# Kernel optimization log

Measured on AMD Instinct MI355X. Metric: run time of the kernel, lower is better.

Reference implementation:

```python
import jax, jax.numpy as jnp
import numpy as np

B, T = 16384, 79
DIMS = [(1, 64), (64, 32), (32, 16), (16, 8), (8, 16), (16, 32), (32, 64), (64, 79)]


def _simple_rnn(x, Wx, Wh, b, act, return_seq):
    # x: [B, T, D] -> SimpleRNN: h_t = act(x_t @ Wx + h_{t-1} @ Wh + b)
    xb = jnp.einsum('btd,du->btu', x, Wx) + b  # precompute input projection
    h0 = jnp.zeros((x.shape[0], Wh.shape[0]), x.dtype)

    def step(h, xt):
        h = act(xt + h @ Wh)
        return h, h

    hT, hs = jax.lax.scan(step, h0, jnp.swapaxes(xb, 0, 1))  # scan over time
    return jnp.swapaxes(hs, 0, 1) if return_seq else hT


def setup_inputs() -> dict:
    key = jax.random.key(0)
    ks = jax.random.split(key, 3 * len(DIMS) + 1)
    inp = {"x": jax.random.normal(ks[0], (B, T), dtype=jnp.float32)}
    for i, (d, u) in enumerate(DIMS):
        inp[f"Wx{i}"] = jax.random.normal(ks[1 + 3 * i], (d, u), dtype=jnp.float32) / np.sqrt(d).astype(np.float32)
        inp[f"Wh{i}"] = jax.random.normal(ks[2 + 3 * i], (u, u), dtype=jnp.float32) / np.sqrt(u).astype(np.float32)
        inp[f"b{i}"] = jnp.zeros((u,), dtype=jnp.float32)
    return inp


def reference(x, Wx0, Wh0, b0, Wx1, Wh1, b1, Wx2, Wh2, b2, Wx3, Wh3, b3,
              Wx4, Wh4, b4, Wx5, Wh5, b5, Wx6, Wh6, b6, Wx7, Wh7, b7):
    params = [(Wx0, Wh0, b0), (Wx1, Wh1, b1), (Wx2, Wh2, b2), (Wx3, Wh3, b3),
              (Wx4, Wh4, b4), (Wx5, Wh5, b5), (Wx6, Wh6, b6), (Wx7, Wh7, b7)]
    h = x[..., None]  # [B, T, 1]  (tf.expand_dims(x, -1))
    n = len(params)
    for i, (Wx, Wh, b) in enumerate(params):
        last = i == n - 1
        act = jax.nn.sigmoid if last else jax.nn.relu
        h = _simple_rnn(h, Wx, Wh, b, act, return_seq=not last)
    return h  # decoded: [B, 79]
```

## Files before the change

### kernel.cpp

```cpp
#include <hip/hip_runtime.h>
#include <hip/hip_bf16.h>

#define DEVFN static __device__ __forceinline__

typedef short bf16x8 __attribute__((ext_vector_type(8)));
typedef float f32x4  __attribute__((ext_vector_type(4)));

constexpr int TSEQ  = 79;
constexpr int NSTEP = TSEQ + 7;
constexpr int MWG   = 16;
constexpr int ROWU  = 344;
constexpr int NBLK  = 16384 / MWG;

constexpr int LD[8]   = {1,64,32,16,8,16,32,64};
constexpr int LU[8]   = {64,32,16,8,16,32,64,79};
constexpr int LS[8]   = {0,8,72,104,120,128,144,176};
constexpr int LO[8]   = {8,72,104,120,128,144,176,240};
constexpr int LKP[8]  = {96,96,64,32,32,64,96,160};
constexpr int LKS[8]  = {3,3,2,1,1,2,3,5};
constexpr int LUP[8]  = {64,32,16,16,16,32,64,80};
constexpr int WOFF[8] = {0,6144,9216,10240,10752,11264,13312,19456};
constexpr int WTOTAL  = 32256;

constexpr int WNG[4]     = {1,2,4,2};
constexpr int WGL[4][4]  = {{7,0,0,0},{7,1,0,0},{0,2,3,4},{6,5,0,0}};
constexpr int WGT0[4][4] = {{0,0,0,0},{3,0,0,0},{0,0,0,0},{0,0,0,0}};
constexpr int WGNT[4][4] = {{3,0,0,0},{2,2,0,0},{4,1,1,1},{4,2,0,0}};

DEVFN unsigned short f2bf(float f) {
  unsigned int u = __builtin_bit_cast(unsigned int, f);
  unsigned int r = (u + 0x7FFFu + ((u >> 16) & 1u)) >> 16;
  return (unsigned short)r;
}
DEVFN unsigned int pkbf(float a, float b) {
#if __has_builtin(__builtin_amdgcn_cvt_pk_bf16_f32)
  auto r = __builtin_amdgcn_cvt_pk_bf16_f32(a, b);
  static_assert(sizeof(r) == 4, "v2bf16 expected");
  return __builtin_bit_cast(unsigned int, r);
#else
  return (unsigned)f2bf(a) | ((unsigned)f2bf(b) << 16);
#endif
}
DEVFN float sigmoidf(float v) { return 1.0f / (1.0f + __expf(-v)); }

__global__ void __launch_bounds__(256) prep_weights(
    const float* Wx0, const float* Wh0, const float* Wx1, const float* Wh1,
    const float* Wx2, const float* Wh2, const float* Wx3, const float* Wh3,
    const float* Wx4, const float* Wh4, const float* Wx5, const float* Wh5,
    const float* Wx6, const float* Wh6, const float* Wx7, const float* Wh7,
    unsigned short* __restrict__ wt)
{
  const float* wxp[8] = {Wx0,Wx1,Wx2,Wx3,Wx4,Wx5,Wx6,Wx7};
  const float* whp[8] = {Wh0,Wh1,Wh2,Wh3,Wh4,Wh5,Wh6,Wh7};
  int idx = blockIdx.x * 256 + threadIdx.x;
  if (idx >= WTOTAL) return;
#pragma unroll
  for (int l = 0; l < 8; ++l) {
    int sz = LUP[l] * LKP[l];
    if (idx >= WOFF[l] && idx < WOFF[l] + sz) {
      int local = idx - WOFF[l];
      int j = local / LKP[l];
      int k = local - j * LKP[l];
      float v = 0.f;
      if (j < LU[l]) {
        if (l == 0) {
          if (k == 0) v = Wx0[j];
          else if (k >= 8 && k < 72) v = Wh0[(k - 8) * 64 + j];
        } else {
          if (k < LD[l]) v = wxp[l][k * LU[l] + j];
          else if (k < LD[l] + LU[l]) v = whp[l][(k - LD[l]) * LU[l] + j];
        }
      }
      wt[idx] = f2bf(v);
    }
  }
}

template <int W>
DEVFN void preload(const unsigned short* __restrict__ wt, int lane, bf16x8 (&af)[16])
{
  const int m0 = lane & 15, quad = lane >> 4;
  int ai = 0;
#pragma unroll
  for (int g = 0; g < 4; ++g) {
    if (g >= WNG[W]) break;
    const int l = WGL[W][g], t0 = WGT0[W][g], nt = WGNT[W][g];
    const int ks = LKS[l], Kp = LKP[l];
#pragma unroll
    for (int t = 0; t < 4; ++t) {
      if (t >= nt) continue;
      const int j = (t0 + t) * 16 + m0;
      const unsigned short* base = wt + WOFF[l] + j * Kp;
#pragma unroll
      for (int k = 0; k < 5; ++k) {
        if (k >= ks) continue;
        af[ai + t * ks + k] = *reinterpret_cast<const bf16x8*>(base + k * 32 + quad * 8);
      }
    }
    ai += nt * ks;
  }
}

template <int W>
DEVFN void step(int s, const unsigned short (*rb)[ROWU], unsigned short (*wb)[ROWU],
                const bf16x8 (&af)[16], const float (*bl)[80],
                const unsigned short (*xl)[80], float* __restrict__ out,
                int bb, int lane)
{
  const int m = lane & 15, quad = lane >> 4;
  int ai = 0;
#pragma unroll
  for (int g = 0; g < 4; ++g) {
    if (g >= WNG[W]) break;
    const int l = WGL[W][g], t0 = WGT0[W][g], nt = WGNT[W][g];
    const int ks = LKS[l], S = LS[l], O = LO[l], u = LU[l];
    if (s >= l && s <= l + TSEQ - 1) {
      f32x4 acc[4];
#pragma unroll
      for (int t = 0; t < 4; ++t)
        if (t < nt)
          acc[t] = *reinterpret_cast<const f32x4*>(&bl[l][(t0 + t) * 16 + quad * 4]);
#pragma unroll
      for (int k = 0; k < 5; ++k) {
        if (k >= ks) break;
        bf16x8 bf = *reinterpret_cast<const bf16x8*>(&rb[m][S + k * 32 + quad * 8]);
#pragma unroll
        for (int t = 0; t < 4; ++t)
          if (t < nt)
            acc[t] = __builtin_amdgcn_mfma_f32_16x16x32_bf16(af[ai + t * ks + k], bf, acc[t], 0, 0, 0);
      }
#pragma unroll
      for (int t = 0; t < 4; ++t) {
        if (t >= nt) continue;
        const int jb = (t0 + t) * 16 + quad * 4;
        float v0 = acc[t][0], v1 = acc[t][1], v2 = acc[t][2], v3 = acc[t][3];
        if (l == 7) {
          v0 = sigmoidf(v0); v1 = sigmoidf(v1); v2 = sigmoidf(v2); v3 = sigmoidf(v3);
          if (s == NSTEP - 1) {
            float* op = out + (size_t)(bb + m) * 79 + jb;
            if (jb + 0 < 79) op[0] = v0;
            if (jb + 1 < 79) op[1] = v1;
            if (jb + 2 < 79) op[2] = v2;
            if (jb + 3 < 79) op[3] = v3;
          } else {
            uint2 pk;
            pk.x = pkbf(v0, v1);
            pk.y = pkbf(v2, v3);
            *reinterpret_cast<uint2*>(&wb[m][O + jb]) = pk;
          }
        } else {
          if (jb < u) {
            v0 = fmaxf(v0, 0.f); v1 = fmaxf(v1, 0.f); v2 = fmaxf(v2, 0.f); v3 = fmaxf(v3, 0.f);
            uint2 pk;
            pk.x = pkbf(v0, v1);
            pk.y = pkbf(v2, v3);
            *reinterpret_cast<uint2*>(&wb[m][O + jb]) = pk;
          }
        }
      }
    }
    ai += nt * ks;
  }
  if constexpr (W == 0) {
    if (lane < MWG && s < TSEQ - 1) {
      wb[lane][0] = xl[lane][s + 1];
    }
  }
}

__global__ void __launch_bounds__(256)
__attribute__((amdgpu_waves_per_eu(4, 4)))
rnn_wavefront(
    const float* __restrict__ x, const unsigned short* __restrict__ wt,
    const float* b0, const float* b1, const float* b2, const float* b3,
    const float* b4, const float* b5, const float* b6, const float* b7,
    float* __restrict__ out)
{
  __shared__ __align__(16) unsigned short hbuf[2][MWG][ROWU];
  __shared__ __align__(16) float          bl[8][80];
  __shared__ __align__(4)  unsigned short xl[MWG][80];
  const int tid = threadIdx.x, lane = tid & 63, wid = tid >> 6;
  const int bb = blockIdx.x * MWG;
  const float* bptr[8] = {b0, b1, b2, b3, b4, b5, b6, b7};

  {
    unsigned int* p = (unsigned int*)&hbuf[0][0][0];
    constexpr int NW = 2 * MWG * ROWU / 2;
    for (int i = tid; i < NW; i += 256) p[i] = 0;
  }
  for (int i = tid; i < 8 * 80; i += 256) {
    int l = i / 80, j = i - l * 80;
    bl[l][j] = (j < LU[l]) ? bptr[l][j] : 0.0f;
  }
  {
    const float* xb = x + (size_t)bb * TSEQ;
    for (int i = tid; i < MWG * TSEQ; i += 256) {
      int r = i / TSEQ, c = i - r * TSEQ;
      xl[r][c] = f2bf(xb[i]);
    }
  }
  __syncthreads();
  if (tid < MWG) hbuf[0][tid][0] = xl[tid][0];

  bf16x8 af[16];
  if (wid == 0)      preload<0>(wt, lane, af);
  else if (wid == 1) preload<1>(wt, lane, af);
  else if (wid == 2) preload<2>(wt, lane, af);
  else               preload<3>(wt, lane, af);
  __syncthreads();

  for (int s = 0; s < NSTEP; ++s) {
    const unsigned short (*rb)[ROWU] = hbuf[s & 1];
    unsigned short (*wb)[ROWU]       = hbuf[(s + 1) & 1];
    if (wid == 0)      step<0>(s, rb, wb, af, bl, xl, out, bb, lane);
    else if (wid == 1) step<1>(s, rb, wb, af, bl, xl, out, bb, lane);
    else if (wid == 2) step<2>(s, rb, wb, af, bl, xl, out, bb, lane);
    else               step<3>(s, rb, wb, af, bl, xl, out, bb, lane);
    __syncthreads();
  }
}

extern "C" void kernel_launch(void* const* d_in, const int* in_sizes, int n_in,
                              void* d_out, int out_size, void* d_ws, size_t ws_size,
                              hipStream_t stream)
{
  const float* x = (const float*)d_in[0];
  const float* Wx[8]; const float* Wh[8]; const float* b[8];
  for (int i = 0; i < 8; ++i) {
    Wx[i] = (const float*)d_in[1 + 3 * i];
    Wh[i] = (const float*)d_in[2 + 3 * i];
    b[i]  = (const float*)d_in[3 + 3 * i];
  }
  unsigned short* wt = (unsigned short*)d_ws;

  prep_weights<<<(WTOTAL + 255) / 256, 256, 0, stream>>>(
      Wx[0], Wh[0], Wx[1], Wh[1], Wx[2], Wh[2], Wx[3], Wh[3],
      Wx[4], Wh[4], Wx[5], Wh[5], Wx[6], Wh[6], Wx[7], Wh[7], wt);

  rnn_wavefront<<<NBLK, 256, 0, stream>>>(
      x, wt, b[0], b[1], b[2], b[3], b[4], b[5], b[6], b[7], (float*)d_out);
}
```

Before: 255.9 us.

## Collapse wavefront RNN into a single wave per block holding all weights

The kernel goes from four waves per block, with layers split across waves and a block barrier every time step, to one 64-lane wave that runs all eight layers each step. All layer weights (63 bf16x8 fragments) and biases sit in registers, and the launch is pinned to one wave per EU. This removes the per-step __syncthreads and the uneven work split across waves. In exchange there are fewer resident waves per SIMD to hide MFMA and LDS latency, and register pressure is very high.

```diff
diff --git a/kernel.cpp b/kernel.cpp
--- a/kernel.cpp
+++ b/kernel.cpp
@@ -19,13 +19,11 @@
 constexpr int LKP[8]  = {96,96,64,32,32,64,96,160};
 constexpr int LKS[8]  = {3,3,2,1,1,2,3,5};
 constexpr int LUP[8]  = {64,32,16,16,16,32,64,80};
+constexpr int LTI[8]  = {4,2,1,1,1,2,4,5};
 constexpr int WOFF[8] = {0,6144,9216,10240,10752,11264,13312,19456};
 constexpr int WTOTAL  = 32256;
-
-constexpr int WNG[4]     = {1,2,4,2};
-constexpr int WGL[4][4]  = {{7,0,0,0},{7,1,0,0},{0,2,3,4},{6,5,0,0}};
-constexpr int WGT0[4][4] = {{0,0,0,0},{3,0,0,0},{0,0,0,0},{0,0,0,0}};
-constexpr int WGNT[4][4] = {{3,0,0,0},{2,2,0,0},{4,1,1,1},{4,2,0,0}};
+constexpr int AFOFF[8] = {0,12,18,20,21,22,26,38};
+constexpr int BTOFF[8] = {0,4,6,7,8,9,11,15};
 
 DEVFN unsigned short f2bf(float f) {
   unsigned int u = __builtin_bit_cast(unsigned int, f);
@@ -76,147 +74,129 @@
   }
 }
 
-template <int W>
-DEVFN void preload(const unsigned short* __restrict__ wt, int lane, bf16x8 (&af)[16])
-{
-  const int m0 = lane & 15, quad = lane >> 4;
-  int ai = 0;
-#pragma unroll
-  for (int g = 0; g < 4; ++g) {
-    if (g >= WNG[W]) break;
-    const int l = WGL[W][g], t0 = WGT0[W][g], nt = WGNT[W][g];
-    const int ks = LKS[l], Kp = LKP[l];
-#pragma unroll
-    for (int t = 0; t < 4; ++t) {
-      if (t >= nt) continue;
-      const int j = (t0 + t) * 16 + m0;
-      const unsigned short* base = wt + WOFF[l] + j * Kp;
-#pragma unroll
-      for (int k = 0; k < 5; ++k) {
-        if (k >= ks) continue;
-        af[ai + t * ks + k] = *reinterpret_cast<const bf16x8*>(base + k * 32 + quad * 8);
+template <int L>
+DEVFN void layer_step(int s, const unsigned short* __restrict__ rb,
+                      unsigned short* __restrict__ wb,
+                      const bf16x8 (&af)[63], const f32x4 (&bi)[20],
+                      float* __restrict__ out, int bb, int m, int quad)
+{
+  if (s < L || s > L + TSEQ - 1) return;
+  constexpr int ks = LKS[L], S = LS[L], O = LO[L], u = LU[L];
+  constexpr int nt = LTI[L], AF = AFOFF[L], BT = BTOFF[L];
+
+  bf16x8 bf[5];
+#pragma unroll
+  for (int k = 0; k < ks; ++k)
+    bf[k] = *reinterpret_cast<const bf16x8*>(&rb[m * ROWU + S + k * 32 + quad * 8]);
+
+  f32x4 acc[5];
+#pragma unroll
+  for (int t = 0; t < nt; ++t) acc[t] = bi[BT + t];
+#pragma unroll
+  for (int k = 0; k < ks; ++k)
+#pragma unroll
+    for (int t = 0; t < nt; ++t)
+      acc[t] = __builtin_amdgcn_mfma_f32_16x16x32_bf16(af[AF + t * ks + k], bf[k], acc[t], 0, 0, 0);
+
+#pragma unroll
+  for (int t = 0; t < nt; ++t) {
+    const int jb = t * 16 + quad * 4;
+    float v0 = acc[t][0], v1 = acc[t][1], v2 = acc[t][2], v3 = acc[t][3];
+    if (L == 7) {
+      v0 = sigmoidf(v0); v1 = sigmoidf(v1); v2 = sigmoidf(v2); v3 = sigmoidf(v3);
+      if (s == NSTEP - 1) {
+        float* op = out + (size_t)(bb + m) * 79 + jb;
+        if (jb + 0 < 79) op[0] = v0;
+        if (jb + 1 < 79) op[1] = v1;
+        if (jb + 2 < 79) op[2] = v2;
+        if (jb + 3 < 79) op[3] = v3;
+      } else {
+        uint2 pk;
+        pk.x = pkbf(v0, v1);
+        pk.y = pkbf(v2, v3);
+        *reinterpret_cast<uint2*>(&wb[m * ROWU + O + jb]) = pk;
       }
-    }
-    ai += nt * ks;
-  }
-}
-
-template <int W>
-DEVFN void step(int s, const unsigned short (*rb)[ROWU], unsigned short (*wb)[ROWU],
-                const bf16x8 (&af)[16], const float (*bl)[80],
-                const unsigned short (*xl)[80], float* __restrict__ out,
-                int bb, int lane)
-{
-  const int m = lane & 15, quad = lane >> 4;
-  int ai = 0;
-#pragma unroll
-  for (int g = 0; g < 4; ++g) {
-    if (g >= WNG[W]) break;
-    const int l = WGL[W][g], t0 = WGT0[W][g], nt = WGNT[W][g];
-    const int ks = LKS[l], S = LS[l], O = LO[l], u = LU[l];
-    if (s >= l && s <= l + TSEQ - 1) {
-      f32x4 acc[4];
-#pragma unroll
-      for (int t = 0; t < 4; ++t)
-        if (t < nt)
-          acc[t] = *reinterpret_cast<const f32x4*>(&bl[l][(t0 + t) * 16 + quad * 4]);
-#pragma unroll
-      for (int k = 0; k < 5; ++k) {
-        if (k >= ks) break;
-        bf16x8 bf = *reinterpret_cast<const bf16x8*>(&rb[m][S + k * 32 + quad * 8]);
-#pragma unroll
-        for (int t = 0; t < 4; ++t)
-          if (t < nt)
-            acc[t] = __builtin_amdgcn_mfma_f32_16x16x32_bf16(af[ai + t * ks + k], bf, acc[t], 0, 0, 0);
-      }
-#pragma unroll
-      for (int t = 0; t < 4; ++t) {
-        if (t >= nt) continue;
-        const int jb = (t0 + t) * 16 + quad * 4;
-        float v0 = acc[t][0], v1 = acc[t][1], v2 = acc[t][2], v3 = acc[t][3];
-        if (l == 7) {
-          v0 = sigmoidf(v0); v1 = sigmoidf(v1); v2 = sigmoidf(v2); v3 = sigmoidf(v3);
-          if (s == NSTEP - 1) {
-            float* op = out + (size_t)(bb + m) * 79 + jb;
-            if (jb + 0 < 79) op[0] = v0;
-            if (jb + 1 < 79) op[1] = v1;
-            if (jb + 2 < 79) op[2] = v2;
-            if (jb + 3 < 79) op[3] = v3;
-          } else {
-            uint2 pk;
-            pk.x = pkbf(v0, v1);
-            pk.y = pkbf(v2, v3);
-            *reinterpret_cast<uint2*>(&wb[m][O + jb]) = pk;
-          }
-        } else {
-          if (jb < u) {
-            v0 = fmaxf(v0, 0.f); v1 = fmaxf(v1, 0.f); v2 = fmaxf(v2, 0.f); v3 = fmaxf(v3, 0.f);
-            uint2 pk;
-            pk.x = pkbf(v0, v1);
-            pk.y = pkbf(v2, v3);
-            *reinterpret_cast<uint2*>(&wb[m][O + jb]) = pk;
-          }
-        }
-      }
-    }
-    ai += nt * ks;
-  }
-  if constexpr (W == 0) {
-    if (lane < MWG && s < TSEQ - 1) {
-      wb[lane][0] = xl[lane][s + 1];
-    }
-  }
-}
-
-__global__ void __launch_bounds__(256)
-__attribute__((amdgpu_waves_per_eu(4, 4)))
-rnn_wavefront(
+    } else if (jb < u) {
+      v0 = fmaxf(v0, 0.f); v1 = fmaxf(v1, 0.f); v2 = fmaxf(v2, 0.f); v3 = fmaxf(v3, 0.f);
+      uint2 pk;
+      pk.x = pkbf(v0, v1);
+      pk.y = pkbf(v2, v3);
+      *reinterpret_cast<uint2*>(&wb[m * ROWU + O + jb]) = pk;
+    }
+  }
+}
+
+__global__ void __launch_bounds__(64)
+__attribute__((amdgpu_waves_per_eu(1, 1)))
+rnn_sw(
     const float* __restrict__ x, const unsigned short* __restrict__ wt,
     const float* b0, const float* b1, const float* b2, const float* b3,
     const float* b4, const float* b5, const float* b6, const float* b7,
     float* __restrict__ out)
 {
-  __shared__ __align__(16) unsigned short hbuf[2][MWG][ROWU];
+  constexpr int HHALF = MWG * ROWU;
+  __shared__ __align__(16) unsigned short hbuf[2 * HHALF];
   __shared__ __align__(16) float          bl[8][80];
   __shared__ __align__(4)  unsigned short xl[MWG][80];
-  const int tid = threadIdx.x, lane = tid & 63, wid = tid >> 6;
+  const int lane = threadIdx.x;
+  const int m = lane & 15, quad = lane >> 4;
   const int bb = blockIdx.x * MWG;
   const float* bptr[8] = {b0, b1, b2, b3, b4, b5, b6, b7};
 
   {
-    unsigned int* p = (unsigned int*)&hbuf[0][0][0];
-    constexpr int NW = 2 * MWG * ROWU / 2;
-    for (int i = tid; i < NW; i += 256) p[i] = 0;
-  }
-  for (int i = tid; i < 8 * 80; i += 256) {
+    unsigned int* p = (unsigned int*)&hbuf[0];
+    for (int i = lane; i < HHALF; i += 64) p[i] = 0;
+  }
+  for (int i = lane; i < 8 * 80; i += 64) {
     int l = i / 80, j = i - l * 80;
     bl[l][j] = (j < LU[l]) ? bptr[l][j] : 0.0f;
   }
   {
     const float* xb = x + (size_t)bb * TSEQ;
-    for (int i = tid; i < MWG * TSEQ; i += 256) {
+    for (int i = lane; i < MWG * TSEQ; i += 64) {
       int r = i / TSEQ, c = i - r * TSEQ;
       xl[r][c] = f2bf(xb[i]);
     }
   }
   __syncthreads();
-  if (tid < MWG) hbuf[0][tid][0] = xl[tid][0];
-
-  bf16x8 af[16];
-  if (wid == 0)      preload<0>(wt, lane, af);
-  else if (wid == 1) preload<1>(wt, lane, af);
-  else if (wid == 2) preload<2>(wt, lane, af);
-  else               preload<3>(wt, lane, af);
-  __syncthreads();
+  if (lane < MWG) hbuf[lane * ROWU] = xl[lane][0];
+
+  f32x4 bi[20];
+#pragma unroll
+  for (int l = 0; l < 8; ++l)
+#pragma unroll
+    for (int t = 0; t < 5; ++t)
+      if (t < LTI[l])
+        bi[BTOFF[l] + t] = *reinterpret_cast<const f32x4*>(&bl[l][t * 16 + quad * 4]);
+
+  bf16x8 af[63];
+#pragma unroll
+  for (int l = 0; l < 8; ++l) {
+#pragma unroll
+    for (int t = 0; t < 5; ++t) {
+      if (t >= LTI[l]) continue;
+      const unsigned short* base = wt + WOFF[l] + (t * 16 + m) * LKP[l];
+#pragma unroll
+      for (int k = 0; k < 5; ++k)
+        if (k < LKS[l])
+          af[AFOFF[l] + t * LKS[l] + k] =
+              *reinterpret_cast<const bf16x8*>(base + k * 32 + quad * 8);
+    }
+  }
 
   for (int s = 0; s < NSTEP; ++s) {
-    const unsigned short (*rb)[ROWU] = hbuf[s & 1];
-    unsigned short (*wb)[ROWU]       = hbuf[(s + 1) & 1];
-    if (wid == 0)      step<0>(s, rb, wb, af, bl, xl, out, bb, lane);
-    else if (wid == 1) step<1>(s, rb, wb, af, bl, xl, out, bb, lane);
-    else if (wid == 2) step<2>(s, rb, wb, af, bl, xl, out, bb, lane);
-    else               step<3>(s, rb, wb, af, bl, xl, out, bb, lane);
-    __syncthreads();
+    const unsigned short* rb = hbuf + (s & 1) * HHALF;
+    unsigned short*       wb = hbuf + ((s + 1) & 1) * HHALF;
+    layer_step<0>(s, rb, wb, af, bi, out, bb, m, quad);
+    layer_step<1>(s, rb, wb, af, bi, out, bb, m, quad);
+    layer_step<2>(s, rb, wb, af, bi, out, bb, m, quad);
+    layer_step<3>(s, rb, wb, af, bi, out, bb, m, quad);
+    layer_step<4>(s, rb, wb, af, bi, out, bb, m, quad);
+    layer_step<5>(s, rb, wb, af, bi, out, bb, m, quad);
+    layer_step<6>(s, rb, wb, af, bi, out, bb, m, quad);
+    layer_step<7>(s, rb, wb, af, bi, out, bb, m, quad);
+    if (lane < MWG && s < TSEQ - 1)
+      wb[lane * ROWU] = xl[lane][s + 1];
   }
 }
 
@@ -237,6 +217,6 @@
       Wx[0], Wh[0], Wx[1], Wh[1], Wx[2], Wh[2], Wx[3], Wh[3],
       Wx[4], Wh[4], Wx[5], Wh[5], Wx[6], Wh[6], Wx[7], Wh[7], wt);
 
-  rnn_wavefront<<<NBLK, 256, 0, stream>>>(
+  rnn_sw<<<NBLK, 64, 0, stream>>>(
       x, wt, b[0], b[1], b[2], b[3], b[4], b[5], b[6], b[7], (float*)d_out);
 }
```

New measurement: 344.0 us. +34.4%, slower.
